# Performance work log

Measured on AMD Instinct MI355X. Metric: run time of the kernel, lower is better.

The kernel has to match this reference:

```python
import jax, jax.numpy as jnp
import numpy as np

B_SZ, SEQ, CH, ORDER = 8, 8192, 256, 64
EPS_LN = 1e-5
EPS_H = 1e-6


def setup_inputs() -> dict:
    key = jax.random.key(0)
    ks = jax.random.split(key, 12)
    s = 1.0 / np.sqrt(CH)
    x = jax.random.normal(ks[0], (B_SZ, SEQ, CH), jnp.float32)
    # RTF params: A = denominator coeffs (monic, leading 1 implied), B = numerator coeffs
    A = 0.01 * jax.random.normal(ks[1], (CH, ORDER), jnp.float32)  # small -> stable 1/A(z)
    Bp = 0.1 * jax.random.normal(ks[2], (CH, ORDER), jnp.float32)
    h0 = jnp.zeros((1,), jnp.float32)  # init torch.tensor([0.])
    W_enc = s * jax.random.normal(ks[3], (CH, CH), jnp.float32)
    b_enc = jnp.zeros((CH,), jnp.float32)
    W_fc = s * jax.random.normal(ks[4], (CH, CH), jnp.float32)
    b_fc = jnp.zeros((CH,), jnp.float32)
    gamma = jnp.ones((CH,), jnp.float32)
    beta = jnp.zeros((CH,), jnp.float32)
    W_dec = s * jax.random.normal(ks[5], (CH, CH), jnp.float32)
    b_dec = jnp.zeros((CH,), jnp.float32)
    return {"x": x, "A": A, "Bp": Bp, "h0": h0, "W_enc": W_enc, "b_enc": b_enc,
            "W_fc": W_fc, "b_fc": b_fc, "gamma": gamma, "beta": beta,
            "W_dec": W_dec, "b_dec": b_dec}


def _rtf_kernel(A, Bp, L):
    # K(z) = B(z)/A(z) with monic denominator a = [1, A_1..A_order]
    C = A.shape[0]
    a = jnp.concatenate([jnp.ones((C, 1), A.dtype), A], axis=1)  # (C, order+1)
    af = jnp.fft.rfft(a, n=L, axis=1)
    bf = jnp.fft.rfft(Bp, n=L, axis=1)
    return jnp.fft.irfft(bf / af, n=L, axis=1)  # (C, L)


def _causal_fft_conv(x, K):
    # x: (B, L, C); K: (C, L) per-channel causal filter
    L = x.shape[1]
    n = 2 * L
    xf = jnp.fft.rfft(x, n=n, axis=1)            # (B, n/2+1, C)
    Kf = jnp.fft.rfft(K.T, n=n, axis=0)          # (n/2+1, C)
    return jnp.fft.irfft(xf * Kf[None], n=n, axis=1)[:, :L]


def reference(x, A, Bp, h0, W_enc, b_enc, W_fc, b_fc, gamma, beta, W_dec, b_dec):
    gelu = lambda t: jax.nn.gelu(t, approximate=False)
    xe = x @ W_enc.T + b_enc                      # encode
    L = xe.shape[1]
    K = _rtf_kernel(A, Bp, L)                     # kernel generation from (A,B)
    h1 = _causal_fft_conv(xe, K)                  # FFT long convolution
    y1 = gelu(h1 + h0 * xe)                       # SSMRTF output (mult_activation=gelu)
    y2 = gelu(y1 @ W_fc.T + b_fc)                 # fc + final_act
    y2 = y2 + xe                                  # skip
    mu = jnp.mean(y2, axis=-1, keepdims=True)     # LayerNorm over channels
    var = jnp.mean(jnp.square(y2 - mu), axis=-1, keepdims=True)
    y2 = (y2 - mu) * jax.lax.rsqrt(var + EPS_LN) * gamma + beta
    y = y2 @ W_dec.T + b_dec                      # decode
    # h = ||y||_inf over seq / ||x_enc||_inf over seq
    h = jnp.max(jnp.abs(y), axis=1) / (jnp.max(jnp.abs(xe), axis=1) + EPS_H)
    return (y, h)
```

## Files before the change

### kernel.cpp

```cpp
#include <hip/hip_runtime.h>
#include <math.h>


#define BSZ   8
#define SEQ   8192
#define CHN   256
#define ORD   64
#define STAPS 512
#define NDD   17
#define PREPAD 544
#define XROW  (PREPAD + SEQ)
#define MTOT  (BSZ * SEQ)
#define YELEMS (MTOT * CHN)

#define CT     2048
#define CROWE  3072

typedef short s16x8 __attribute__((ext_vector_type(8)));
typedef float f32x4 __attribute__((ext_vector_type(4)));

#define MFMA16(a, b, c) __builtin_amdgcn_mfma_f32_16x16x32_bf16((a), (b), (c), 0, 0, 0)

__device__ __forceinline__ void gll16(const void* g, void* l) {
  __builtin_amdgcn_global_load_lds(
      (const __attribute__((address_space(1))) unsigned int*)g,
      (__attribute__((address_space(3))) unsigned int*)l, 16, 0, 0);
}

#define PERMC(row, h) (((row) * 8 + ((h) ^ ((row) & 7))) * 8)

__device__ __forceinline__ unsigned short f2bf(float f) {
  unsigned u = __float_as_uint(f);
  return (unsigned short)((u + 0x7FFFu + ((u >> 16) & 1u)) >> 16);
}
__device__ __forceinline__ float bf2f(unsigned short h) {
  return __uint_as_float(((unsigned)h) << 16);
}
__device__ __forceinline__ float geluf(float x) {
  float x2 = x * x;
  float y = x * __builtin_fmaf(0.0356774081f, x2, 0.7978845608f);
  float e = __builtin_amdgcn_exp2f(-2.8853900818f * y);
  return x * __builtin_amdgcn_rcpf(1.0f + e);
}
__device__ __forceinline__ uint4 packbf8(float4 a, float4 b) {
  uint4 r;
  r.x = (unsigned)f2bf(a.x) | ((unsigned)f2bf(a.y) << 16);
  r.y = (unsigned)f2bf(a.z) | ((unsigned)f2bf(a.w) << 16);
  r.z = (unsigned)f2bf(b.x) | ((unsigned)f2bf(b.y) << 16);
  r.w = (unsigned)f2bf(b.z) | ((unsigned)f2bf(b.w) << 16);
  return r;
}

__global__ __launch_bounds__(256) void k_pz(const float* we, const float* wf,
                                            const float* wd, unsigned short* owe,
                                            unsigned short* owf, unsigned short* owd,
                                            unsigned short* xeT, uint4* maxbufs) {
  int bx = blockIdx.x, tid = threadIdx.x;
  if (bx < 768) {
    int i = bx * 256 + tid;
    int which = i >> 16, off = i & 65535;
    if (which == 0)      owe[off] = f2bf(we[off]);
    else if (which == 1) owf[off] = f2bf(wf[off]);
    else                 owd[off] = f2bf(wd[off]);
  } else {
    int i = (bx - 768) * 256 + tid;
    uint4 z; z.x = 0; z.y = 0; z.z = 0; z.w = 0;
    if (i < 2048 * 68) {
      int row = i / 68, cc = i % 68;
      *(uint4*)((char*)xeT + (size_t)row * (XROW * 2) + (size_t)cc * 16) = z;
    } else {
      int j = i - 2048 * 68;
      if (j < 1024) maxbufs[j] = z;
    }
  }
}

__device__ __forceinline__ void kgen_body(char* smem, const float* A, const float* Bp,
                                          unsigned short* afr, int blk) {
  int tid = threadIdx.x, lane = tid & 63;
  int wv = tid >> 6;
  int c = blk * 4 + wv;
  float* base = (float*)smem + wv * 1280;
  float* Gsp = base;
  float* Et  = base + 576;
  float* Asl = base + 640;
  float* Bsl = base + 704;
  float* Kb  = base + 768;

  Asl[lane] = A[(size_t)c * ORD + lane];
  Bsl[lane] = Bp[(size_t)c * ORD + lane];
#pragma unroll
  for (int k = 0; k < 9; ++k) Gsp[k * 64 + lane] = 0.f;
  if (lane == 0) Gsp[64] = 1.f;

  for (int n = 1; n < STAPS; n <<= 1) {
    float e0 = 0.f, e1 = 0.f, e2 = 0.f, e3 = 0.f;
#pragma unroll
    for (int u = 1; u <= 64; u += 4) {
      e0 += Asl[u - 1] * Gsp[64 + n + lane - u];
      e1 += Asl[u]     * Gsp[63 + n + lane - u];
      e2 += Asl[u + 1] * Gsp[62 + n + lane - u];
      e3 += Asl[u + 2] * Gsp[61 + n + lane - u];
    }
    Et[lane] = (e0 + e1) + (e2 + e3);
    int nk = (n + 63) >> 6;
    for (int k = 0; k < nk; ++k) {
      int idx = k * 64 + lane;
      float a0 = 0.f, a1 = 0.f, a2 = 0.f, a3 = 0.f;
#pragma unroll
      for (int i = 0; i < 64; i += 4) {
        a0 += Et[i]     * Gsp[64 + idx - i];
        a1 += Et[i + 1] * Gsp[63 + idx - i];
        a2 += Et[i + 2] * Gsp[62 + idx - i];
        a3 += Et[i + 3] * Gsp[61 + idx - i];
      }
      if (idx < n) Gsp[64 + n + idx] = -((a0 + a1) + (a2 + a3));
    }
  }

  for (int k = 0; k < 8; ++k) {
    int t = k * 64 + lane;
    float a0 = 0.f, a1 = 0.f, a2 = 0.f, a3 = 0.f;
#pragma unroll
    for (int j = 0; j < 64; j += 4) {
      a0 += Bsl[j]     * Gsp[64 + t - j];
      a1 += Bsl[j + 1] * Gsp[63 + t - j];
      a2 += Bsl[j + 2] * Gsp[62 + t - j];
      a3 += Bsl[j + 3] * Gsp[61 + t - j];
    }
    Kb[t] = (a0 + a1) + (a2 + a3);
  }

  int m = lane & 15, quad = lane >> 4;
  for (int dd = 0; dd < NDD; ++dd) {
    unsigned short v[8];
#pragma unroll
    for (int j = 0; j < 8; ++j) {
      int k = quad * 8 + j;
      int d = 2 * dd + (k >> 4);
      int p = k & 15;
      int s = 16 * d + m - p;
      float kv = (s >= 0 && s < STAPS) ? Kb[s] : 0.f;
      v[j] = f2bf(kv);
    }
    uint4 pk;
    pk.x = (unsigned)v[0] | ((unsigned)v[1] << 16);
    pk.y = (unsigned)v[2] | ((unsigned)v[3] << 16);
    pk.z = (unsigned)v[4] | ((unsigned)v[5] << 16);
    pk.w = (unsigned)v[6] | ((unsigned)v[7] << 16);
    *(uint4*)(afr + ((size_t)(c * NDD + dd) * 64 + lane) * 8) = pk;
  }
}

__global__ __launch_bounds__(256) void k_g1k(const float* A, const float* Bp,
                                             unsigned short* afr,
                                             const float* x, const unsigned short* wb,
                                             const float* benc, unsigned short* xeT,
                                             unsigned int* maxxe) {
  __shared__ __align__(16) char smem[40960];
  if (blockIdx.x < 64) {
    kgen_body(smem, A, Bp, afr, blockIdx.x);
    return;
  }
  unsigned short* As = (unsigned short*)smem;
  unsigned short* Bs = (unsigned short*)(smem + 32768);
  int tid = threadIdx.x, lane = tid & 63, wv = tid >> 6;
  int ln15 = lane & 15, hf = lane >> 4;
  size_t t0 = (size_t)(blockIdx.x - 64) * 64;
  int b = (int)(t0 >> 13), tin = (int)(t0 & 8191);
  f32x4 acc[4][4];
#pragma unroll
  for (int i = 0; i < 4; ++i)
#pragma unroll
    for (int j = 0; j < 4; ++j) { acc[i][j][0]=0.f; acc[i][j][1]=0.f; acc[i][j][2]=0.f; acc[i][j][3]=0.f; }

  for (int k0 = 0; k0 < CHN; k0 += 64) {
    __syncthreads();
#pragma unroll
    for (int i = 0; i < 8; ++i) {
      int p = 512 * wv + 64 * i + lane;
      int row = p >> 3, h = (p & 7) ^ (row & 7);
      gll16(wb + (size_t)row * CHN + k0 + h * 8, &As[(512 * wv + 64 * i) * 8]);
    }
    {
      int row = tid >> 2, hb = (tid & 3) * 2;
      const float* src = x + (t0 + row) * CHN + k0 + hb * 8;
      float4 f0 = *(const float4*)src;
      float4 f1 = *(const float4*)(src + 4);
      float4 f2 = *(const float4*)(src + 8);
      float4 f3 = *(const float4*)(src + 12);
      *(uint4*)&Bs[PERMC(row, hb)]     = packbf8(f0, f1);
      *(uint4*)&Bs[PERMC(row, hb + 1)] = packbf8(f2, f3);
    }
    __syncthreads();
#pragma unroll
    for (int ks = 0; ks < 2; ++ks) {
      s16x8 af[4], bfr[4];
#pragma unroll
      for (int mt = 0; mt < 4; ++mt) {
        int row = 64 * wv + 16 * mt + ln15;
        af[mt] = *(const s16x8*)&As[PERMC(row, ks * 4 + hf)];
      }
#pragma unroll
      for (int nt = 0; nt < 4; ++nt) {
        int row = 16 * nt + ln15;
        bfr[nt] = *(const s16x8*)&Bs[PERMC(row, ks * 4 + hf)];
      }
#pragma unroll
      for (int mt = 0; mt < 4; ++mt)
#pragma unroll
        for (int nt = 0; nt < 4; ++nt)
          acc[mt][nt] = MFMA16(af[mt], bfr[nt], acc[mt][nt]);
    }
  }
  int quad = hf;
#pragma unroll
  for (int mt = 0; mt < 4; ++mt) {
#pragma unroll
    for (int r = 0; r < 4; ++r) {
      int row = 64 * wv + 16 * mt + 4 * quad + r;
      float bias = benc[row];
      float mv = 0.f;
#pragma unroll
      for (int nt = 0; nt < 4; ++nt) {
        float v = acc[mt][nt][r] + bias;
        int t = tin + 16 * nt + ln15;
        xeT[(size_t)(b * CHN + row) * XROW + PREPAD + t] = f2bf(v);
        mv = fmaxf(mv, fabsf(v));
      }
      mv = fmaxf(mv, __shfl_xor(mv, 1)); mv = fmaxf(mv, __shfl_xor(mv, 2));
      mv = fmaxf(mv, __shfl_xor(mv, 4)); mv = fmaxf(mv, __shfl_xor(mv, 8));
      if (ln15 == 0) atomicMax(&maxxe[b * CHN + row], __float_as_uint(mv));
    }
  }
}

__global__ __launch_bounds__(256) void k_conv(const unsigned short* xeT,
                                              const unsigned short* afr,
                                              unsigned short* y1, const float* h0p) {
  __shared__ __align__(16) unsigned short xet[4 * CROWE];
  __shared__ __align__(16) unsigned short bnc[4 * CT];
  int tid = threadIdx.x, lane = tid & 63, wv = tid >> 6;
  int idx = blockIdx.x;
  int tg = idx & 3, cg = (idx >> 2) & 63, b = idx >> 8;
  int c0 = cg * 4, t0 = tg * CT;
  int c = c0 + wv;

  s16x8 afrg[NDD];
  {
    const unsigned short* ap = afr + (size_t)c * (NDD * 512) + (size_t)lane * 8;
#pragma unroll
    for (int dd = 0; dd < NDD; ++dd)
      afrg[dd] = *(const s16x8*)(ap + (size_t)dd * 512);
  }
  {
    int lp = lane ^ ((lane >> 3) & 7);
    const unsigned short* gbase = xeT + (size_t)(b * CHN + c) * XROW + t0;
    unsigned short* lbase = &xet[wv * CROWE];
#pragma unroll
    for (int k = 0; k < 6; ++k)
      gll16(gbase + (size_t)(64 * k + lp) * 8, &lbase[k * 64 * 8]);
  }
  float h0 = h0p[0];

  int n = lane & 15, quad = lane >> 4;
  int qc = quad - ((quad >> 1) << 2);
  const char* xb = (const char*)&xet[wv * CROWE];

  int ad[NDD];
  {
    int cb0 = 2 * n + qc + 68;
#pragma unroll
    for (int dd = 0; dd < NDD; ++dd) {
      int cc = cb0 - 4 * dd;
      ad[dd] = (cc ^ ((cc >> 3) & 7)) * 16;
    }
  }
  int ead;
  {
    int ch = 68 + 2 * n + (quad >> 1);
    ead = (ch ^ ((ch >> 3) & 7)) * 16 + 8 * (quad & 1);
  }
  __syncthreads();

#pragma unroll 1
  for (int s = 0; s < 8; ++s) {
    f32x4 a0, a1;
    a0[0]=0.f; a0[1]=0.f; a0[2]=0.f; a0[3]=0.f;
    a1[0]=0.f; a1[1]=0.f; a1[2]=0.f; a1[3]=0.f;
#pragma unroll
    for (int dd = 0; dd < 16; dd += 2) {
      a0 = MFMA16(afrg[dd],     *(const s16x8*)(xb + ad[dd]),     a0);
      a1 = MFMA16(afrg[dd + 1], *(const s16x8*)(xb + ad[dd + 1]), a1);
    }
    a0 = MFMA16(afrg[16], *(const s16x8*)(xb + ad[16]), a0);
    uint2 xvp = *(const uint2*)(xb + ead);
    unsigned short o[4];
#pragma unroll
    for (int r = 0; r < 4; ++r) {
      float xv = bf2f(((const unsigned short*)&xvp)[r]);
      float v = (a0[r] + a1[r]) + h0 * xv;
      o[r] = f2bf(geluf(v));
    }
    uint2 pw;
    pw.x = (unsigned)o[0] | ((unsigned)o[1] << 16);
    pw.y = (unsigned)o[2] | ((unsigned)o[3] << 16);
    *(uint2*)&bnc[wv * CT + 256 * s + 16 * n + 4 * quad] = pw;
#pragma unroll
    for (int dd = 16; dd >= 8; --dd) ad[dd] = ad[dd - 8];
#pragma unroll
    for (int dd = 0; dd < 8; ++dd) ad[dd] = (ad[dd] + 512) ^ 64;
    ead = (ead + 512) ^ 64;
  }
  __syncthreads();
  {
    const size_t obase = (size_t)(b * SEQ + t0) * CHN + c0;
#pragma unroll
    for (int s = 0; s < 8; ++s) {
      int tl = 256 * s + tid;
      uint2 pk;
      pk.x = (unsigned)bnc[tl] | ((unsigned)bnc[CT + tl] << 16);
      pk.y = (unsigned)bnc[2 * CT + tl] | ((unsigned)bnc[3 * CT + tl] << 16);
      *(uint2*)(y1 + obase + (size_t)tl * CHN) = pk;
    }
  }
}

__global__ __launch_bounds__(256) void k_gemm2(const unsigned short* y1,
                                               const unsigned short* wb, const float* bfc,
                                               const unsigned short* xeT, const float* gam,
                                               const float* bet, unsigned short* y2n) {
  __shared__ __align__(16) unsigned short Ws[256 * 64];
  __shared__ __align__(16) unsigned short Asb[64 * 64];
  __shared__ float pl[64][2][2];
  int tid = threadIdx.x, lane = tid & 63, wv = tid >> 6;
  int ln15 = lane & 15, hf = lane >> 4, quad = hf;
  size_t M0 = (size_t)blockIdx.x * 64;
  int b = (int)(M0 >> 13), tin = (int)(M0 & 8191);
  int mh = wv & 1, nh = wv >> 1;
  f32x4 acc[2][8];
#pragma unroll
  for (int i = 0; i < 2; ++i)
#pragma unroll
    for (int j = 0; j < 8; ++j) { acc[i][j][0]=0.f; acc[i][j][1]=0.f; acc[i][j][2]=0.f; acc[i][j][3]=0.f; }

  for (int k0 = 0; k0 < CHN; k0 += 64) {
    __syncthreads();
#pragma unroll
    for (int i = 0; i < 8; ++i) {
      int p = 512 * wv + 64 * i + lane;
      int row = p >> 3, h = (p & 7) ^ (row & 7);
      gll16(wb + (size_t)row * CHN + k0 + h * 8, &Ws[(512 * wv + 64 * i) * 8]);
    }
#pragma unroll
    for (int i = 0; i < 2; ++i) {
      int p = 128 * wv + 64 * i + lane;
      int row = p >> 3, h = (p & 7) ^ (row & 7);
      gll16(y1 + (M0 + row) * CHN + k0 + h * 8, &Asb[(128 * wv + 64 * i) * 8]);
    }
    __syncthreads();
#pragma unroll
    for (int ks = 0; ks < 2; ++ks) {
      s16x8 af[2], bfr[8];
#pragma unroll
      for (int mt = 0; mt < 2; ++mt) {
        int row = 32 * mh + 16 * mt + ln15;
        af[mt] = *(const s16x8*)&Asb[PERMC(row, ks * 4 + hf)];
      }
#pragma unroll
      for (int nt = 0; nt < 8; ++nt) {
        int row = 128 * nh + 16 * nt + ln15;
        bfr[nt] = *(const s16x8*)&Ws[PERMC(row, ks * 4 + hf)];
      }
#pragma unroll
      for (int mt = 0; mt < 2; ++mt)
#pragma unroll
        for (int nt = 0; nt < 8; ++nt)
          acc[mt][nt] = MFMA16(af[mt], bfr[nt], acc[mt][nt]);
    }
  }
  float g8[8], be8[8], bf8[8];
#pragma unroll
  for (int nt = 0; nt < 8; ++nt) {
    int col = 128 * nh + 16 * nt + ln15;
    g8[nt] = gam[col]; be8[nt] = bet[col]; bf8[nt] = bfc[col];
  }
#pragma unroll
  for (int mt = 0; mt < 2; ++mt) {
    int mlb = 32 * mh + 16 * mt + 4 * quad;
    uint2 xv2[8];
#pragma unroll
    for (int nt = 0; nt < 8; ++nt) {
      int col = 128 * nh + 16 * nt + ln15;
      xv2[nt] = *(const uint2*)(xeT + (size_t)(b * CHN + col) * XROW + PREPAD + tin + mlb);
    }
#pragma unroll
    for (int r = 0; r < 4; ++r) {
      int ml = mlb + r;
      float s1 = 0.f, s2 = 0.f;
#pragma unroll
      for (int nt = 0; nt < 8; ++nt) {
        float t2 = acc[mt][nt][r] + bf8[nt];
        float xv = bf2f(((const unsigned short*)&xv2[nt])[r]);
        float y2 = geluf(t2) + xv;
        acc[mt][nt][r] = y2;
        s1 += y2; s2 += y2 * y2;
      }
      s1 += __shfl_xor(s1, 1); s2 += __shfl_xor(s2, 1);
      s1 += __shfl_xor(s1, 2); s2 += __shfl_xor(s2, 2);
      s1 += __shfl_xor(s1, 4); s2 += __shfl_xor(s2, 4);
      s1 += __shfl_xor(s1, 8); s2 += __shfl_xor(s2, 8);
      if (ln15 == 0) { pl[ml][nh][0] = s1; pl[ml][nh][1] = s2; }
    }
  }
  __syncthreads();
#pragma unroll
  for (int mt = 0; mt < 2; ++mt) {
#pragma unroll
    for (int r = 0; r < 4; ++r) {
      int ml = 32 * mh + 16 * mt + 4 * quad + r;
      float s1 = pl[ml][0][0] + pl[ml][1][0];
      float s2 = pl[ml][0][1] + pl[ml][1][1];
      float mu = s1 * (1.f / 256.f);
      float var = s2 * (1.f / 256.f) - mu * mu;
      float ri = rsqrtf(var + 1e-5f);
#pragma unroll
      for (int nt = 0; nt < 8; ++nt) {
        int col = 128 * nh + 16 * nt + ln15;
        float yn = (acc[mt][nt][r] - mu) * ri * g8[nt] + be8[nt];
        y2n[(M0 + ml) * CHN + col] = f2bf(yn);
      }
    }
  }
}

__global__ __launch_bounds__(256) void k_gemm3(const unsigned short* y2n,
                                               const unsigned short* wb, const float* bd,
                                               float* yout, unsigned int* maxy) {
  __shared__ __align__(16) unsigned short Ws[256 * 64];
  __shared__ __align__(16) unsigned short Asb[64 * 64];
  int tid = threadIdx.x, lane = tid & 63, wv = tid >> 6;
  int ln15 = lane & 15, hf = lane >> 4, quad = hf;
  size_t M0 = (size_t)blockIdx.x * 64;
  int b = (int)(M0 >> 13);
  int mh = wv & 1, nh = wv >> 1;
  f32x4 acc[2][8];
#pragma unroll
  for (int i = 0; i < 2; ++i)
#pragma unroll
    for (int j = 0; j < 8; ++j) { acc[i][j][0]=0.f; acc[i][j][1]=0.f; acc[i][j][2]=0.f; acc[i][j][3]=0.f; }

  for (int k0 = 0; k0 < CHN; k0 += 64) {
    __syncthreads();
#pragma unroll
    for (int i = 0; i < 8; ++i) {
      int p = 512 * wv + 64 * i + lane;
      int row = p >> 3, h = (p & 7) ^ (row & 7);
      gll16(wb + (size_t)row * CHN + k0 + h * 8, &Ws[(512 * wv + 64 * i) * 8]);
    }
#pragma unroll
    for (int i = 0; i < 2; ++i) {
      int p = 128 * wv + 64 * i + lane;
      int row = p >> 3, h = (p & 7) ^ (row & 7);
      gll16(y2n + (M0 + row) * CHN + k0 + h * 8, &Asb[(128 * wv + 64 * i) * 8]);
    }
    __syncthreads();
#pragma unroll
    for (int ks = 0; ks < 2; ++ks) {
      s16x8 af[2], bfr[8];
#pragma unroll
      for (int mt = 0; mt < 2; ++mt) {
        int row = 32 * mh + 16 * mt + ln15;
        af[mt] = *(const s16x8*)&Asb[PERMC(row, ks * 4 + hf)];
      }
#pragma unroll
      for (int nt = 0; nt < 8; ++nt) {
        int row = 128 * nh + 16 * nt + ln15;
        bfr[nt] = *(const s16x8*)&Ws[PERMC(row, ks * 4 + hf)];
      }
#pragma unroll
      for (int mt = 0; mt < 2; ++mt)
#pragma unroll
        for (int nt = 0; nt < 8; ++nt)
          acc[mt][nt] = MFMA16(af[mt], bfr[nt], acc[mt][nt]);
    }
  }
  float bd8[8];
#pragma unroll
  for (int nt = 0; nt < 8; ++nt) bd8[nt] = bd[128 * nh + 16 * nt + ln15];
#pragma unroll
  for (int mt = 0; mt < 2; ++mt)
#pragma unroll
    for (int r = 0; r < 4; ++r) {
      int ml = 32 * mh + 16 * mt + 4 * quad + r;
#pragma unroll
      for (int nt = 0; nt < 8; ++nt) {
        int col = 128 * nh + 16 * nt + ln15;
        float v = acc[mt][nt][r] + bd8[nt];
        acc[mt][nt][r] = v;
        yout[(M0 + ml) * CHN + col] = v;
      }
    }
#pragma unroll
  for (int nt = 0; nt < 8; ++nt) {
    int col = 128 * nh + 16 * nt + ln15;
    float mv = 0.f;
#pragma unroll
    for (int mt = 0; mt < 2; ++mt)
#pragma unroll
      for (int r = 0; r < 4; ++r) mv = fmaxf(mv, fabsf(acc[mt][nt][r]));
    mv = fmaxf(mv, __shfl_xor(mv, 16));
    mv = fmaxf(mv, __shfl_xor(mv, 32));
    if (quad == 0) atomicMax(&maxy[b * CHN + col], __float_as_uint(mv));
  }
}

__global__ __launch_bounds__(256) void k_hfin(const unsigned int* maxxe,
                                              const unsigned int* maxy, float* hout) {
  int i = blockIdx.x * 256 + threadIdx.x;
  if (i < BSZ * CHN) {
    float mx = __uint_as_float(maxxe[i]);
    float my = __uint_as_float(maxy[i]);
    hout[i] = my / (mx + 1e-6f);
  }
}

extern "C" void kernel_launch(void* const* d_in, const int* in_sizes, int n_in,
                              void* d_out, int out_size, void* d_ws, size_t ws_size,
                              hipStream_t stream) {
  const float* x   = (const float*)d_in[0];
  const float* A   = (const float*)d_in[1];
  const float* Bp  = (const float*)d_in[2];
  const float* h0  = (const float*)d_in[3];
  const float* We  = (const float*)d_in[4];
  const float* be  = (const float*)d_in[5];
  const float* Wf  = (const float*)d_in[6];
  const float* bfc = (const float*)d_in[7];
  const float* gam = (const float*)d_in[8];
  const float* bet = (const float*)d_in[9];
  const float* Wd  = (const float*)d_in[10];
  const float* bd  = (const float*)d_in[11];

  char* ws = (char*)d_ws;
  unsigned short* y1  = (unsigned short*)(ws + 0);
  unsigned short* afr = (unsigned short*)(ws + 33554432);
  unsigned short* web = (unsigned short*)(ws + 38010880);
  unsigned short* wfb = (unsigned short*)(ws + 38141952);
  unsigned short* wdb = (unsigned short*)(ws + 38273024);
  unsigned int*  maxxe = (unsigned int*)(ws + 38404096);
  unsigned int*  maxy  = (unsigned int*)(ws + 38412288);

  unsigned short* xeT = (unsigned short*)d_out;
  float* yout = (float*)d_out;
  float* hout = yout + YELEMS;

  k_pz<<<1316, 256, 0, stream>>>(We, Wf, Wd, web, wfb, wdb, xeT, (uint4*)maxxe);
  k_g1k<<<1088, 256, 0, stream>>>(A, Bp, afr, x, web, be, xeT, maxxe);
  k_conv<<<2048, 256, 0, stream>>>(xeT, afr, y1, h0);
  k_gemm2<<<1024, 256, 0, stream>>>(y1, wfb, bfc, xeT, gam, bet, y1);
  k_gemm3<<<1024, 256, 0, stream>>>(y1, wdb, bd, yout, maxy);
  k_hfin<<<8, 256, 0, stream>>>(maxxe, maxy, hout);
}
```

Before: 299.7 us.

## Move kernel generation into prep kernel and vectorize its LDS reads

Kernel-coefficient generation moves out of the first GEMM launch and into the weight-conversion/zeroing prep kernel, which now uses 512-thread blocks with 8 channels per block. The GEMM1 kernel no longer carries the long serial kgen blocks that could delay its tail. Kgen keeps two copies of G offset by one element so the reversed-index convolution can use aligned float2/float4 LDS loads instead of scalar ones. The cost is more LDS per block and double writes of each G value.

```diff
diff --git a/kernel.cpp b/kernel.cpp
--- a/kernel.cpp
+++ b/kernel.cpp
@@ -51,82 +51,79 @@
   return r;
 }
 
-__global__ __launch_bounds__(256) void k_pz(const float* we, const float* wf,
-                                            const float* wd, unsigned short* owe,
-                                            unsigned short* owf, unsigned short* owd,
-                                            unsigned short* xeT, uint4* maxbufs) {
-  int bx = blockIdx.x, tid = threadIdx.x;
-  if (bx < 768) {
-    int i = bx * 256 + tid;
-    int which = i >> 16, off = i & 65535;
-    if (which == 0)      owe[off] = f2bf(we[off]);
-    else if (which == 1) owf[off] = f2bf(wf[off]);
-    else                 owd[off] = f2bf(wd[off]);
-  } else {
-    int i = (bx - 768) * 256 + tid;
-    uint4 z; z.x = 0; z.y = 0; z.z = 0; z.w = 0;
-    if (i < 2048 * 68) {
-      int row = i / 68, cc = i % 68;
-      *(uint4*)((char*)xeT + (size_t)row * (XROW * 2) + (size_t)cc * 16) = z;
-    } else {
-      int j = i - 2048 * 68;
-      if (j < 1024) maxbufs[j] = z;
-    }
-  }
-}
-
-__device__ __forceinline__ void kgen_body(char* smem, const float* A, const float* Bp,
-                                          unsigned short* afr, int blk) {
-  int tid = threadIdx.x, lane = tid & 63;
-  int wv = tid >> 6;
-  int c = blk * 4 + wv;
-  float* base = (float*)smem + wv * 1280;
-  float* Gsp = base;
-  float* Et  = base + 576;
-  float* Asl = base + 640;
-  float* Bsl = base + 704;
-  float* Kb  = base + 768;
+__device__ __forceinline__ void kgen8(float* smemk, const float* A, const float* Bp,
+                                      unsigned short* afr, int blk) {
+  int tid = threadIdx.x, lane = tid & 63, wv = tid >> 6;
+  int c = blk * 8 + wv;
+  float* base = smemk + wv * 1872;
+  float* G0 = base;
+  float* G1 = base + 584;
+  float* Et = base + 1168;
+  float* Asl = base + 1232;
+  float* Bsl = base + 1296;
+  float* Kb = base + 1360;
 
   Asl[lane] = A[(size_t)c * ORD + lane];
   Bsl[lane] = Bp[(size_t)c * ORD + lane];
-#pragma unroll
-  for (int k = 0; k < 9; ++k) Gsp[k * 64 + lane] = 0.f;
-  if (lane == 0) Gsp[64] = 1.f;
+  for (int i = lane; i < 1168; i += 64) base[i] = 0.f;
+  if (lane == 0) { G0[64] = 1.f; G1[65] = 1.f; }
 
   for (int n = 1; n < STAPS; n <<= 1) {
+    int par = (n + lane) & 1;
+    const float* Gc = par ? G1 : G0;
+    int I0 = 64 + n + lane + par;
     float e0 = 0.f, e1 = 0.f, e2 = 0.f, e3 = 0.f;
 #pragma unroll
-    for (int u = 1; u <= 64; u += 4) {
-      e0 += Asl[u - 1] * Gsp[64 + n + lane - u];
-      e1 += Asl[u]     * Gsp[63 + n + lane - u];
-      e2 += Asl[u + 1] * Gsp[62 + n + lane - u];
-      e3 += Asl[u + 2] * Gsp[61 + n + lane - u];
+    for (int g = 0; g < 16; ++g) {
+      float4 av = *(const float4*)&Asl[4 * g];
+      float2 vA = *(const float2*)&Gc[I0 - 4 * g - 2];
+      float2 vB = *(const float2*)&Gc[I0 - 4 * g - 4];
+      e0 += av.x * vA.y;
+      e1 += av.y * vA.x;
+      e2 += av.z * vB.y;
+      e3 += av.w * vB.x;
     }
     Et[lane] = (e0 + e1) + (e2 + e3);
     int nk = (n + 63) >> 6;
     for (int k = 0; k < nk; ++k) {
       int idx = k * 64 + lane;
+      int parU = (idx + 1) & 1;
+      const float* Gu = parU ? G1 : G0;
+      int J0 = 64 + idx - 1 + parU;
       float a0 = 0.f, a1 = 0.f, a2 = 0.f, a3 = 0.f;
 #pragma unroll
-      for (int i = 0; i < 64; i += 4) {
-        a0 += Et[i]     * Gsp[64 + idx - i];
-        a1 += Et[i + 1] * Gsp[63 + idx - i];
-        a2 += Et[i + 2] * Gsp[62 + idx - i];
-        a3 += Et[i + 3] * Gsp[61 + idx - i];
-      }
-      if (idx < n) Gsp[64 + n + idx] = -((a0 + a1) + (a2 + a3));
+      for (int g = 0; g < 16; ++g) {
+        float4 ev = *(const float4*)&Et[4 * g];
+        float2 vA = *(const float2*)&Gu[J0 - 4 * g];
+        float2 vB = *(const float2*)&Gu[J0 - 4 * g - 2];
+        a0 += ev.x * vA.y;
+        a1 += ev.y * vA.x;
+        a2 += ev.z * vB.y;
+        a3 += ev.w * vB.x;
+      }
+      if (idx < n) {
+        float gv = -((a0 + a1) + (a2 + a3));
+        G0[64 + n + idx] = gv;
+        G1[65 + n + idx] = gv;
+      }
     }
   }
 
   for (int k = 0; k < 8; ++k) {
     int t = k * 64 + lane;
+    int parB = (t + 1) & 1;
+    const float* Gb = parB ? G1 : G0;
+    int J0 = 64 + t - 1 + parB;
     float a0 = 0.f, a1 = 0.f, a2 = 0.f, a3 = 0.f;
 #pragma unroll
-    for (int j = 0; j < 64; j += 4) {
-      a0 += Bsl[j]     * Gsp[64 + t - j];
-      a1 += Bsl[j + 1] * Gsp[63 + t - j];
-      a2 += Bsl[j + 2] * Gsp[62 + t - j];
-      a3 += Bsl[j + 3] * Gsp[61 + t - j];
+    for (int g = 0; g < 16; ++g) {
+      float4 bv = *(const float4*)&Bsl[4 * g];
+      float2 vA = *(const float2*)&Gb[J0 - 4 * g];
+      float2 vB = *(const float2*)&Gb[J0 - 4 * g - 2];
+      a0 += bv.x * vA.y;
+      a1 += bv.y * vA.x;
+      a2 += bv.z * vB.y;
+      a3 += bv.w * vB.x;
     }
     Kb[t] = (a0 + a1) + (a2 + a3);
   }
@@ -152,21 +149,44 @@
   }
 }
 
-__global__ __launch_bounds__(256) void k_g1k(const float* A, const float* Bp,
+__global__ __launch_bounds__(512) void k_pzk(const float* A, const float* Bp,
                                              unsigned short* afr,
-                                             const float* x, const unsigned short* wb,
-                                             const float* benc, unsigned short* xeT,
-                                             unsigned int* maxxe) {
-  __shared__ __align__(16) char smem[40960];
-  if (blockIdx.x < 64) {
-    kgen_body(smem, A, Bp, afr, blockIdx.x);
+                                             const float* we, const float* wf,
+                                             const float* wd, unsigned short* owe,
+                                             unsigned short* owf, unsigned short* owd,
+                                             unsigned short* xeT, uint4* maxbufs) {
+  __shared__ __align__(16) float smemk[8 * 1872];
+  int bx = blockIdx.x, tid = threadIdx.x;
+  if (bx < 32) {
+    kgen8(smemk, A, Bp, afr, bx);
     return;
   }
-  unsigned short* As = (unsigned short*)smem;
-  unsigned short* Bs = (unsigned short*)(smem + 32768);
+  int i = (bx - 32) * 512 + tid;
+  if (i < 196608) {
+    int which = i >> 16, off = i & 65535;
+    if (which == 0)      owe[off] = f2bf(we[off]);
+    else if (which == 1) owf[off] = f2bf(wf[off]);
+    else                 owd[off] = f2bf(wd[off]);
+  } else {
+    int j = i - 196608;
+    uint4 z; z.x = 0; z.y = 0; z.z = 0; z.w = 0;
+    if (j < 139264) {
+      int row = j / 68, cc = j % 68;
+      *(uint4*)((char*)xeT + (size_t)row * (XROW * 2) + (size_t)cc * 16) = z;
+    } else {
+      maxbufs[j - 139264] = z;
+    }
+  }
+}
+
+__global__ __launch_bounds__(256) void k_gemm1(const float* x, const unsigned short* wb,
+                                               const float* benc, unsigned short* xeT,
+                                               unsigned int* maxxe) {
+  __shared__ __align__(16) unsigned short As[256 * 64];
+  __shared__ __align__(16) unsigned short Bs[64 * 64];
   int tid = threadIdx.x, lane = tid & 63, wv = tid >> 6;
   int ln15 = lane & 15, hf = lane >> 4;
-  size_t t0 = (size_t)(blockIdx.x - 64) * 64;
+  size_t t0 = (size_t)blockIdx.x * 64;
   int b = (int)(t0 >> 13), tin = (int)(t0 & 8191);
   f32x4 acc[4][4];
 #pragma unroll
@@ -554,8 +574,9 @@
   float* yout = (float*)d_out;
   float* hout = yout + YELEMS;
 
-  k_pz<<<1316, 256, 0, stream>>>(We, Wf, Wd, web, wfb, wdb, xeT, (uint4*)maxxe);
-  k_g1k<<<1088, 256, 0, stream>>>(A, Bp, afr, x, web, be, xeT, maxxe);
+  k_pzk<<<690, 512, 0, stream>>>(A, Bp, afr, We, Wf, Wd, web, wfb, wdb,
+                                 xeT, (uint4*)maxxe);
+  k_gemm1<<<1024, 256, 0, stream>>>(x, web, be, xeT, maxxe);
   k_conv<<<2048, 256, 0, stream>>>(xeT, afr, y1, h0);
   k_gemm2<<<1024, 256, 0, stream>>>(y1, wfb, bfc, xeT, gam, bet, y1);
   k_gemm3<<<1024, 256, 0, stream>>>(y1, wdb, bd, yout, maxy);
```

New measurement: 306.7 us. 1.02x slower.
